# Performance work log

Hardware: AMD Instinct MI355X
Metric: run time of the kernel (lower is better)

The kernel has to match this reference:

```python
import jax, jax.numpy as jnp
import numpy as np

NUM_BOXES = 16384
NUM_CLASS = 3
CODE_SIZE = 7
NMS_PRE = 1024
NMS_POST = 512
NMS_THRESH = 0.8
EPS = 1e-8


def _cross(a, b):
    return a[..., 0] * b[..., 1] - a[..., 1] * b[..., 0]


def _bev_corners(b5):
    # b5: (..., 5) = (cx, cy, dx, dy, ry) -> corners (..., 4, 2)
    c, s = jnp.cos(b5[..., 4]), jnp.sin(b5[..., 4])
    off = jnp.array([[0.5, 0.5], [-0.5, 0.5], [-0.5, -0.5], [0.5, -0.5]], dtype=b5.dtype)
    lx = b5[..., 2:3] * off[:, 0]  # (..., 4)
    ly = b5[..., 3:4] * off[:, 1]
    cx = b5[..., 0:1] + lx * c[..., None] - ly * s[..., None]
    cy = b5[..., 1:2] + lx * s[..., None] + ly * c[..., None]
    return jnp.stack([cx, cy], axis=-1)


def _points_in_box(p, b5):
    # p: (..., K, 2), b5: (..., 5) -> (..., K) bool (point inside rotated rect)
    c, s = jnp.cos(b5[..., 4:5]), jnp.sin(b5[..., 4:5])
    rel = p - b5[..., None, 0:2]
    qx = rel[..., 0] * c + rel[..., 1] * s
    qy = -rel[..., 0] * s + rel[..., 1] * c
    return (jnp.abs(qx) <= b5[..., 2:3] * 0.5 + 1e-5) & (jnp.abs(qy) <= b5[..., 3:4] * 0.5 + 1e-5)


def _pairwise_bev_iou(b5):
    # b5: (N, 5) -> (N, N) rotated BEV IoU (matches iou3d nms_gpu's BEV IoU)
    a = b5[:, None, :]
    b = b5[None, :, :]
    ca = _bev_corners(a)  # (N,1,4,2)
    cb = _bev_corners(b)  # (1,N,4,2)
    # edge-edge segment intersections: (N,N,4,4)
    a0, da = ca, jnp.roll(ca, -1, axis=-2) - ca
    b0, db = cb, jnp.roll(cb, -1, axis=-2) - cb
    A0, DA = a0[..., :, None, :], da[..., :, None, :]
    B0, DB = b0[..., None, :, :], db[..., None, :, :]
    den = _cross(DA, DB)
    d = B0 - A0
    den_s = jnp.where(jnp.abs(den) > EPS, den, 1.0)
    t = _cross(d, DB) / den_s
    u = _cross(d, DA) / den_s
    ok = (jnp.abs(den) > EPS) & (t >= 0) & (t <= 1) & (u >= 0) & (u <= 1)
    p_ee = A0 + t[..., None] * DA  # (N,N,4,4,2)
    shp = p_ee.shape[:-3]
    p_ee = p_ee.reshape(shp + (16, 2))
    ok = ok.reshape(shp + (16,))
    in_b = _points_in_box(ca, b)  # corners of A inside B: (N,N,4)
    in_a = _points_in_box(cb, a)  # corners of B inside A: (N,N,4)
    pts = jnp.concatenate([p_ee,
                           jnp.broadcast_to(ca, shp + (4, 2)),
                           jnp.broadcast_to(cb, shp + (4, 2))], axis=-2)  # (N,N,24,2)
    msk = jnp.concatenate([ok, in_b, in_a], axis=-1)  # (N,N,24)
    # order candidate vertices by angle around centroid (intersection is convex)
    cnt = jnp.maximum(msk.sum(-1, keepdims=True), 1)
    ctr = (pts * msk[..., None]).sum(-2, keepdims=True) / cnt[..., None]  # (N,N,1,2)
    ang = jnp.arctan2(pts[..., 1] - ctr[..., 1], pts[..., 0] - ctr[..., 0])
    ang = jnp.where(msk, ang, 1e9)  # invalid points sorted to the end
    order = jnp.argsort(ang, axis=-1)
    pts_s = jnp.take_along_axis(pts, order[..., None], axis=-2)
    msk_s = jnp.take_along_axis(msk, order, axis=-1)
    first = pts_s[..., 0:1, :]
    poly = jnp.where(msk_s[..., None], pts_s, first)  # pad with first vertex (zero shoelace contribution)
    inter = 0.5 * jnp.abs(_cross(poly, jnp.roll(poly, -1, axis=-2)).sum(-1))
    area_a = a[..., 2] * a[..., 3]
    area_b = b[..., 2] * b[..., 3]
    return inter / jnp.maximum(area_a + area_b - inter, 1e-6)


def _greedy_nms(iou, thresh):
    n = iou.shape[0]
    idx = jnp.arange(n)

    def body(i, supp):
        alive = jnp.logical_not(supp[i])
        return supp | (alive & (iou[i] > thresh) & (idx > i))

    supp = jax.lax.fori_loop(0, n, body, jnp.zeros((n,), dtype=bool))
    return ~supp


def _select_one(box_preds, cls_preds):
    # box_preds: (M, 7), cls_preds: (M, C) -> padded selected indices + validity
    scores = jnp.max(cls_preds, axis=1)
    _, top_idx = jax.lax.top_k(scores, NMS_PRE)  # score-descending, like torch.topk
    bev = box_preds[top_idx][:, jnp.array([0, 1, 3, 4, 6])]  # (cx,cy,dx,dy,ry)
    iou = _pairwise_bev_iou(bev)
    keep = _greedy_nms(iou, NMS_THRESH)
    pri = jnp.where(keep, jnp.arange(NMS_PRE), 2 * NMS_PRE)
    pos = jnp.sort(pri)[:NMS_POST]  # kept positions in score order
    valid = pos < NMS_PRE
    sel = top_idx[jnp.minimum(pos, NMS_PRE - 1)]
    return sel, valid


def setup_inputs() -> dict:
    key = jax.random.key(0)
    k1, k2, k3, k4, k5 = jax.random.split(key, 5)
    B = 2
    xy = jax.random.uniform(k1, (B, NUM_BOXES, 2), minval=-50.0, maxval=50.0)
    z = jax.random.uniform(k2, (B, NUM_BOXES, 1), minval=-2.0, maxval=1.0)
    dims = jax.random.uniform(k3, (B, NUM_BOXES, 3), minval=1.0, maxval=5.0)
    ry = jax.random.uniform(k4, (B, NUM_BOXES, 1), minval=-np.pi, maxval=np.pi)
    batch_box_preds = jnp.concatenate([xy, z, dims, ry], axis=-1).astype(jnp.float32)
    batch_cls_preds = (jax.random.normal(k5, (B, NUM_BOXES, NUM_CLASS)) * 3.0).astype(jnp.float32)
    return {"batch_box_preds": batch_box_preds, "batch_cls_preds": batch_cls_preds}


def reference(batch_box_preds, batch_cls_preds):
    # RoIHeadTemplate.proposal_layer: per-sample max-score, class-agnostic NMS,
    # scatter into zero-padded (B, NMS_POST, ...) tensors.
    sel, valid = jax.vmap(_select_one)(batch_box_preds, batch_cls_preds)  # (B, NMS_POST)
    rois = jnp.take_along_axis(batch_box_preds, sel[..., None], axis=1)
    logits = jnp.take_along_axis(batch_cls_preds, sel[..., None], axis=1)
    labels = jnp.argmax(logits, axis=-1)
    scores = jnp.max(logits, axis=-1)
    v = valid[..., None]
    rois = jnp.where(v, rois, 0.0)
    logits = jnp.where(v, logits, 0.0)
    scores = jnp.where(valid, scores, 0.0)
    roi_labels = jnp.where(valid, labels, 0) + 1  # padded slots end up as 1, same as torch (zeros + 1)
    return rois, scores, roi_labels, logits
```

## Files before the change

kernel.cpp:

```cpp
#include <hip/hip_runtime.h>
#include <hip/hip_bf16.h>
#include <math.h>

#define NBOX   16384
#define NPRE   1024
#define NPOST  512
#define NMS_TH 0.8f
#define DEN_EPS 1e-8f
#define NCAND  2048
#define NBUCK  8192
#define SEGCAP 16384
#define HITS_LDS 2048
#define HSPILL  (1u << 19)

typedef unsigned long long ull;

__device__ __forceinline__ unsigned mono_f32(float a) {
  unsigned u = __float_as_uint(a);
  return (u & 0x80000000u) ? ~u : (u | 0x80000000u);
}

__global__ __launch_bounds__(256) void k_sel(
    const float* __restrict__ cls, ull* __restrict__ cand,
    unsigned* __restrict__ candCnt) {
  __shared__ unsigned hist[NBUCK];
  __shared__ unsigned smallu[8];
  __shared__ unsigned thrT, cntL;
  const int b = blockIdx.x >> 3, s = blockIdx.x & 7;
  const int t = threadIdx.x;
  const int lane = t & 63, wv = t >> 6;
  const float* cb = cls + (size_t)b * NBOX * 3;

#pragma unroll
  for (int k = 0; k < NBUCK / 256; ++k) hist[t + k * 256] = 0u;
  if (t == 0) cntL = 0u;
  __syncthreads();

  for (int k = 0; k < 64; ++k) {
    int i = k * 256 + t;
    float sc = fmaxf(cb[i * 3], fmaxf(cb[i * 3 + 1], cb[i * 3 + 2]));
    atomicAdd(&hist[mono_f32(sc) >> 19], 1u);
  }
  __syncthreads();

  unsigned csum = 0;
#pragma unroll 8
  for (int k = 0; k < 32; ++k) csum += hist[t * 32 + k];
  unsigned v = csum;
#pragma unroll
  for (int off = 1; off < 64; off <<= 1) {
    unsigned o = __shfl_down((int)v, off, 64);
    if (lane + off < 64) v += o;
  }
  if (lane == 0) smallu[wv] = v;
  __syncthreads();
  unsigned shi = 0;
  for (int w2 = wv + 1; w2 < 4; ++w2) shi += smallu[w2];
  unsigned incl = v + shi;
  unsigned safter = incl - csum;
  if (safter < NPRE && incl >= NPRE) {
    unsigned c = safter;
    for (int k = 31; k >= 0; --k) {
      c += hist[t * 32 + k];
      if (c >= NPRE) { thrT = (unsigned)(t * 32 + k); break; }
    }
  }
  __syncthreads();
  unsigned T = thrT;

  ull* seg = cand + ((size_t)b * 8 + s) * 2048;
  for (int k = s * 8; k < s * 8 + 8; ++k) {
    int i = k * 256 + t;
    float sc = fmaxf(cb[i * 3], fmaxf(cb[i * 3 + 1], cb[i * 3 + 2]));
    unsigned u = mono_f32(sc);
    bool cnd = (u >> 19) >= T;
    ull bal = __ballot(cnd);
    if (bal) {
      unsigned base = 0;
      if (lane == 0) base = atomicAdd(&cntL, (unsigned)__popcll(bal));
      base = (unsigned)__shfl((int)base, 0, 64);
      if (cnd) {
        unsigned pos = base + (unsigned)__popcll(bal & ((1ull << lane) - 1ull));
        seg[pos] = (((ull)u) << 14) | (ull)(16383 - i);
      }
    }
  }
  __syncthreads();
  if (t == 0) candCnt[b * 8 + s] = cntL;
}

__global__ __launch_bounds__(256) void k_rank(
    const float* __restrict__ box, const ull* __restrict__ cand,
    const unsigned* __restrict__ candCnt,
    int* __restrict__ topi, float* __restrict__ binfo, float4* __restrict__ pinfoG) {
  __shared__ ull candL[NCAND];
  __shared__ unsigned offs[9];
  const int b = blockIdx.x >> 3, g = blockIdx.x & 7;
  const int t = threadIdx.x;

  if (t == 0) {
    unsigned o = 0;
    for (int s = 0; s < 8; ++s) {
      offs[s] = o;
      unsigned c = candCnt[b * 8 + s];
      o += (c < 2048u) ? c : 2048u;
    }
    offs[8] = o;
  }
  __syncthreads();
  unsigned C = offs[8]; if (C > NCAND) C = NCAND;
  for (int s = 0; s < 8; ++s) {
    unsigned base = offs[s], cnt = offs[s + 1] - offs[s];
    const ull* seg = cand + ((size_t)b * 8 + s) * 2048;
    for (unsigned e = (unsigned)t; e < cnt; e += 256) {
      unsigned dst = base + e;
      if (dst < NCAND) candL[dst] = seg[e];
    }
  }
  if (t < 2 && C + t < NCAND) candL[C + t] = 0ull;
  __syncthreads();

  int j = g * 256 + t;
  ull my = ((unsigned)j < C) ? candL[j] : 0ull;
  int r = 0;
  int kmax = (int)((C + 1) >> 1);
  const ulonglong2* p2 = (const ulonglong2*)candL;
  for (int k = 0; k < kmax; ++k) {
    ulonglong2 kk = p2[k];
    r += (kk.x > my) ? 1 : 0;
    r += (kk.y > my) ? 1 : 0;
  }
  if ((unsigned)j >= C || r >= NPRE) return;
  int i = 16383 - (int)(my & 0x3FFFULL);
  topi[b * NPRE + r] = i;
  const float* bp = box + ((size_t)b * NBOX + i) * 7;
  float x = bp[0], y = bp[1], dx = bp[3], dy = bp[4], ry = bp[6];
  float c = cosf(ry), s = sinf(ry);
  float* o = binfo + ((size_t)b * NPRE + r) * 16;
  o[0] = x; o[1] = y; o[2] = dx; o[3] = dy; o[4] = c; o[5] = s;
  const float offx[4] = {0.5f, -0.5f, -0.5f, 0.5f};
  const float offy[4] = {0.5f, 0.5f, -0.5f, -0.5f};
#pragma unroll
  for (int k = 0; k < 4; ++k) {
    float lx = dx * offx[k], ly = dy * offy[k];
    o[6 + k]  = x + lx * c - ly * s;
    o[10 + k] = y + lx * s + ly * c;
  }
  float rad = 0.5f * sqrtf(dx * dx + dy * dy);
  float area = dx * dy;
  o[14] = rad; o[15] = area;
  pinfoG[(size_t)b * NPRE + r] = make_float4(x, y, rad, area);
}

__global__ __launch_bounds__(256) void k_pairs(
    const float4* __restrict__ pinfoG, unsigned* __restrict__ wl,
    unsigned* __restrict__ wlcnt) {
  __shared__ float4 pin[NPRE];
  __shared__ unsigned cntW;
  const int b = blockIdx.x >> 6, blk = blockIdx.x & 63;
  const int t = threadIdx.x;
  const int lane = t & 63, wv = t >> 6;
#pragma unroll
  for (int k = 0; k < 4; ++k) pin[k * 256 + t] = pinfoG[(size_t)b * NPRE + k * 256 + t];
  if (t == 0) cntW = 0u;
  __syncthreads();

  unsigned sbase = ((unsigned)b * 64 + (unsigned)blk) * SEGCAP;
  for (int iter = 0; iter < 64; ++iter) {
    int task = iter * 4 + wv;
    int q = task >> 4, w = task & 15;
    int i = q * 64 + blk;
    if (w * 64 + 63 <= i) continue;
    int j = w * 64 + lane;
    float4 pi = pin[i];
    float4 pj = pin[j];
    bool cnd = false;
    if (j > i) {
      float ddx = pi.x - pj.x, ddy = pi.y - pj.y;
      float rr = pi.z + pj.z + 1e-3f;
      if (ddx * ddx + ddy * ddy <= rr * rr) {
        float mn = fminf(pi.w, pj.w), mx = fmaxf(pi.w, pj.w);
        if (mn > NMS_TH * mx) cnd = true;
      }
    }
    ull bal = __ballot(cnd);
    if (!bal) continue;
    unsigned base = 0;
    if (lane == 0) base = atomicAdd(&cntW, (unsigned)__popcll(bal));
    base = (unsigned)__shfl((int)base, 0, 64);
    if (cnd) {
      unsigned off = base + (unsigned)__popcll(bal & ((1ull << lane) - 1ull));
      wl[sbase + off] = ((unsigned)i << 10) | (unsigned)j;
    }
  }
  __syncthreads();
  if (t == 0) wlcnt[b * 64 + blk] = cntW;
}

__device__ bool iou_exact_gt(const float* __restrict__ Ab, const float* __restrict__ Bb) {
  float ax = Ab[0], ay = Ab[1], bx = Bb[0], by = Bb[1];
  float aA = Ab[15], aB = Bb[15];
  float acx[4], acy[4], bcx[4], bcy[4];
#pragma unroll
  for (int k = 0; k < 4; ++k) {
    acx[k] = Ab[6 + k]; acy[k] = Ab[10 + k];
    bcx[k] = Bb[6 + k]; bcy[k] = Bb[10 + k];
  }
  float px[24], py[24];
  bool act[24];
#pragma unroll
  for (int p = 0; p < 4; ++p) {
    float A0x = acx[p], A0y = acy[p];
    float DAx = acx[(p + 1) & 3] - A0x, DAy = acy[(p + 1) & 3] - A0y;
#pragma unroll
    for (int q = 0; q < 4; ++q) {
      float B0x = bcx[q], B0y = bcy[q];
      float DBx = bcx[(q + 1) & 3] - B0x, DBy = bcy[(q + 1) & 3] - B0y;
      float den = DAx * DBy - DAy * DBx;
      float dxx = B0x - A0x, dyy = B0y - A0y;
      bool dok = fabsf(den) > DEN_EPS;
      float dens = dok ? den : 1.0f;
      float t = (dxx * DBy - dyy * DBx) / dens;
      float u = (dxx * DAy - dyy * DAx) / dens;
      int k = p * 4 + q;
      px[k] = A0x + t * DAx;
      py[k] = A0y + t * DAy;
      act[k] = dok && t >= 0.f && t <= 1.f && u >= 0.f && u <= 1.f;
    }
  }
  float cA = Ab[4], sA = Ab[5], cB = Bb[4], sB = Bb[5];
#pragma unroll
  for (int k = 0; k < 4; ++k) {
    float rx = acx[k] - bx, ry = acy[k] - by;
    float qx =  rx * cB + ry * sB, qy = -rx * sB + ry * cB;
    px[16 + k] = acx[k]; py[16 + k] = acy[k];
    act[16 + k] = (fabsf(qx) <= Bb[2] * 0.5f + 1e-5f) && (fabsf(qy) <= Bb[3] * 0.5f + 1e-5f);
  }
#pragma unroll
  for (int k = 0; k < 4; ++k) {
    float rx = bcx[k] - ax, ry = bcy[k] - ay;
    float qx =  rx * cA + ry * sA, qy = -rx * sA + ry * cA;
    px[20 + k] = bcx[k]; py[20 + k] = bcy[k];
    act[20 + k] = (fabsf(qx) <= Ab[2] * 0.5f + 1e-5f) && (fabsf(qy) <= Ab[3] * 0.5f + 1e-5f);
  }
  int cnt = 0; float sx = 0.f, sy = 0.f;
#pragma unroll
  for (int k = 0; k < 24; ++k)
    if (act[k]) { cnt++; sx += px[k]; sy += py[k]; }
  float fc = (float)(cnt > 1 ? cnt : 1);
  float cx0 = sx / fc, cy0 = sy / fc;
  ull key[24];
#pragma unroll
  for (int k = 0; k < 24; ++k) {
    float ang = atan2f(py[k] - cy0, px[k] - cx0);
    key[k] = act[k] ? ((((ull)mono_f32(ang)) << 5) | (ull)k) : ~0ull;
  }
  ull kmin = ~0ull; float fx = 0.f, fy = 0.f;
#pragma unroll
  for (int k = 0; k < 24; ++k) {
    bool lt = key[k] < kmin;
    kmin = lt ? key[k] : kmin;
    fx = lt ? px[k] : fx;
    fy = lt ? py[k] : fy;
  }
  float ssum = 0.f;
#pragma unroll
  for (int k = 0; k < 24; ++k) {
    ull myk = key[k];
    ull best = ~0ull; float nx = fx, ny = fy;
#pragma unroll
    for (int j = 0; j < 24; ++j) {
      bool c = (key[j] > myk) && (key[j] < best);
      best = c ? key[j] : best;
      nx = c ? px[j] : nx;
      ny = c ? py[j] : ny;
    }
    float contrib = px[k] * ny - py[k] * nx;
    ssum += (myk != ~0ull) ? contrib : 0.f;
  }
  float inter = 0.5f * fabsf(ssum);
  float uni = aA + aB - inter;
  return inter / fmaxf(uni, 1e-6f) > NMS_TH;
}

__device__ __forceinline__ int popbelow(const unsigned* rowbm, int i) {
  int s = 0, w = i >> 5;
  for (int k = 0; k < w; ++k) s += __popc(rowbm[k]);
  s += __popc(rowbm[w] & ((1u << (i & 31)) - 1u));
  return s;
}

__global__ __launch_bounds__(512) void k_fin(
    const float* __restrict__ box, const float* __restrict__ cls,
    const int* __restrict__ topi, const float* __restrict__ binfo,
    const unsigned* __restrict__ wl, const unsigned* __restrict__ wlcnt,
    unsigned* __restrict__ hspill, float* __restrict__ out, int B) {
  __shared__ unsigned maskL[128 * 32];
  __shared__ unsigned hitsL[HITS_LDS];
  __shared__ unsigned rlist[NPRE];
  __shared__ unsigned segoff[65];
  __shared__ unsigned rowbm[32];
  __shared__ ull remv_sh[16];
  __shared__ unsigned smallu[8];
  __shared__ unsigned hcnt, rn_sh;

  const int b = blockIdx.x, t = threadIdx.x;
  const int lane = t & 63, wv = t >> 6;

  for (int k = t; k < 128 * 32; k += 512) maskL[k] = 0u;
  if (t < 32) rowbm[t] = 0u;
  if (t == 0) {
    hcnt = 0u;
    unsigned o = 0;
    for (int s = 0; s < 64; ++s) {
      segoff[s] = o;
      unsigned c = wlcnt[b * 64 + s];
      o += (c < (unsigned)SEGCAP) ? c : (unsigned)SEGCAP;
    }
    segoff[64] = o;
  }
  __syncthreads();

  const float* bi = binfo + (size_t)b * NPRE * 16;
  unsigned W = segoff[64];
  for (unsigned e = (unsigned)t; e < W; e += 512) {
    int lo = 0, hi = 63;
    while (lo < hi) {
      int mid = (lo + hi + 1) >> 1;
      if (segoff[mid] <= e) lo = mid; else hi = mid - 1;
    }
    unsigned pk = wl[((size_t)b * 64 + lo) * SEGCAP + (e - segoff[lo])];
    unsigned i = pk >> 10, j = pk & 1023u;
    if (iou_exact_gt(bi + (size_t)i * 16, bi + (size_t)j * 16)) {
      unsigned h = atomicAdd(&hcnt, 1u);
      if (h < HITS_LDS) hitsL[h] = pk;
      else if (h < HITS_LDS + HSPILL) hspill[(size_t)b * HSPILL + (h - HITS_LDS)] = pk;
      atomicOr(&rowbm[i >> 5], 1u << (i & 31));
    }
  }
  __syncthreads();

  for (int row = t; row < NPRE; row += 512) {
    if ((rowbm[row >> 5] >> (row & 31)) & 1u)
      rlist[popbelow(rowbm, row)] = (unsigned)row;
  }
  if (t == 0) {
    unsigned s = 0;
    for (int w = 0; w < 32; ++w) s += (unsigned)__popc(rowbm[w]);
    rn_sh = s;
  }
  __syncthreads();
  unsigned H = hcnt; if (H > HITS_LDS + HSPILL) H = HITS_LDS + HSPILL;
  for (unsigned h = (unsigned)t; h < H; h += 512) {
    unsigned pk = (h < HITS_LDS) ? hitsL[h] : hspill[(size_t)b * HSPILL + (h - HITS_LDS)];
    unsigned i = pk >> 10, j = pk & 1023u;
    int slot = popbelow(rowbm, (int)i);
    if (slot < 128) atomicOr(&maskL[slot * 32 + (j >> 5)], 1u << (j & 31));
  }
  __syncthreads();

  if (wv == 0) {
    ull remv = 0;
    unsigned rn = rn_sh;
    for (unsigned s = 0; s < rn; ++s) {
      unsigned row = rlist[s];
      ull m = 0;
      if (s < 128) {
        if (lane < 16)
          m = (ull)maskL[s * 32 + lane * 2] | ((ull)maskL[s * 32 + lane * 2 + 1] << 32);
      } else {
        for (unsigned h = 0; h < H; ++h) {
          unsigned pk = (h < HITS_LDS) ? hitsL[h] : hspill[(size_t)b * HSPILL + (h - HITS_LDS)];
          if ((pk >> 10) == row) {
            unsigned j = pk & 1023u;
            if (lane == (int)(j >> 6)) m |= 1ull << (j & 63);
          }
        }
      }
      ull rw = __shfl(remv, (int)(row >> 6), 64);
      if (!((rw >> (row & 63)) & 1ULL)) remv |= m;
    }
    if (lane < 16) remv_sh[lane] = remv;
  }
  __syncthreads();

  int p0 = t * 2;
  ull rw = remv_sh[p0 >> 6];
  int a0 = ((rw >> (p0 & 63)) & 1ULL) ? 0 : 1;
  int a1 = ((rw >> ((p0 + 1) & 63)) & 1ULL) ? 0 : 1;
  int myc = a0 + a1;
  int v = myc;
#pragma unroll
  for (int off = 1; off < 64; off <<= 1) {
    int t2 = __shfl_up(v, off, 64);
    if (lane >= off) v += t2;
  }
  if (lane == 63) smallu[wv] = (unsigned)v;
  __syncthreads();
  int pre = 0;
  for (int w2 = 0; w2 < wv; ++w2) pre += (int)smallu[w2];
  int total = 0;
  for (int w2 = 0; w2 < 8; ++w2) total += (int)smallu[w2];
  int s = pre + v - myc;

  float* rois   = out;
  float* scores = out + (size_t)B * NPOST * 7;
  float* labels = scores + (size_t)B * NPOST;
  float* logits = labels + (size_t)B * NPOST;
  int aa[2] = {a0, a1};
#pragma unroll
  for (int k = 0; k < 2; ++k) {
    if (aa[k] && s < NPOST) {
      int orig = topi[b * NPRE + p0 + k];
      const float* bb = box + ((size_t)b * NBOX + orig) * 7;
      float* ro = rois + ((size_t)b * NPOST + s) * 7;
#pragma unroll
      for (int c2 = 0; c2 < 7; ++c2) ro[c2] = bb[c2];
      const float* cc = cls + ((size_t)b * NBOX + orig) * 3;
      float l0 = cc[0], l1 = cc[1], l2 = cc[2];
      float m = fmaxf(l0, fmaxf(l1, l2));
      int lab = (l0 == m) ? 0 : ((l1 == m) ? 1 : 2);
      scores[b * NPOST + s] = m;
      labels[b * NPOST + s] = (float)(lab + 1);
      float* lg = logits + ((size_t)b * NPOST + s) * 3;
      lg[0] = l0; lg[1] = l1; lg[2] = l2;
    }
    s += aa[k];
  }
  if (t < NPOST && t >= total) {
    float* ro = rois + ((size_t)b * NPOST + t) * 7;
#pragma unroll
    for (int c2 = 0; c2 < 7; ++c2) ro[c2] = 0.f;
    scores[b * NPOST + t] = 0.f;
    labels[b * NPOST + t] = 1.f;
    float* lg = logits + ((size_t)b * NPOST + t) * 3;
    lg[0] = 0.f; lg[1] = 0.f; lg[2] = 0.f;
  }
}

extern "C" void kernel_launch(void* const* d_in, const int* in_sizes, int n_in,
                              void* d_out, int out_size, void* d_ws, size_t ws_size,
                              hipStream_t stream) {
  const float* box = (const float*)d_in[0];
  const float* cls = (const float*)d_in[1];
  float* out = (float*)d_out;
  int B = in_sizes[0] / (NBOX * 7);

  char* w = (char*)d_ws;
  size_t off = 0;
  ull* cand        = (ull*)(w + off);      off += (size_t)B * 8 * 2048 * sizeof(ull);
  unsigned* candCt = (unsigned*)(w + off); off += (size_t)B * 8 * sizeof(unsigned);
  int* topi        = (int*)(w + off);      off += (size_t)B * NPRE * sizeof(int);
  unsigned* wlcnt  = (unsigned*)(w + off); off += (size_t)B * 64 * sizeof(unsigned);
  off = (off + 63) & ~(size_t)63;
  float* binfo     = (float*)(w + off);    off += (size_t)B * NPRE * 16 * sizeof(float);
  float4* pinfoG   = (float4*)(w + off);   off += (size_t)B * NPRE * sizeof(float4);
  unsigned* wl     = (unsigned*)(w + off); off += (size_t)B * 64 * SEGCAP * sizeof(unsigned);
  unsigned* hspill = (unsigned*)(w + off); off += (size_t)B * HSPILL * sizeof(unsigned);
  (void)off; (void)ws_size; (void)out_size; (void)n_in;

  hipLaunchKernelGGL(k_sel,   dim3(B * 8),  dim3(256), 0, stream, cls, cand, candCt);
  hipLaunchKernelGGL(k_rank,  dim3(B * 8),  dim3(256), 0, stream, box, cand, candCt, topi, binfo, pinfoG);
  hipLaunchKernelGGL(k_pairs, dim3(B * 64), dim3(256), 0, stream, pinfoG, wl, wlcnt);
  hipLaunchKernelGGL(k_fin,   dim3(B),      dim3(512), 0, stream, box, cls, topi, binfo, wl, wlcnt, hspill, out, B);
}
```

Measured before the change: 147.7 us.

## Move exact rotated IoU evaluation from per-sample finish kernel into parallel pair kernel

The exact polygon IoU test for candidate pairs now runs in k_pairs, spread over B*64 blocks, instead of in k_fin, which has only one 512-thread block per sample. Candidates are buffered in LDS and evaluated after the scan, and only confirmed hits are written to per-segment global lists. k_fin then reads those hit segments through a binary search over segment offsets to build the row bitmap and suppression masks. The cost is more LDS and register pressure in k_pairs, plus repeated binary searches and global reads in k_fin's fallback path.

```diff
diff --git a/kernel.cpp b/kernel.cpp
--- a/kernel.cpp
+++ b/kernel.cpp
@@ -10,8 +10,7 @@
 #define NCAND  2048
 #define NBUCK  8192
 #define SEGCAP 16384
-#define HITS_LDS 2048
-#define HSPILL  (1u << 19)
+#define CANDL  2048
 
 typedef unsigned long long ull;
 
@@ -152,19 +151,107 @@
   pinfoG[(size_t)b * NPRE + r] = make_float4(x, y, rad, area);
 }
 
+__device__ bool iou_exact_gt(const float* __restrict__ Ab, const float* __restrict__ Bb) {
+  float ax = Ab[0], ay = Ab[1], bx = Bb[0], by = Bb[1];
+  float aA = Ab[15], aB = Bb[15];
+  float acx[4], acy[4], bcx[4], bcy[4];
+#pragma unroll
+  for (int k = 0; k < 4; ++k) {
+    acx[k] = Ab[6 + k]; acy[k] = Ab[10 + k];
+    bcx[k] = Bb[6 + k]; bcy[k] = Bb[10 + k];
+  }
+  float px[24], py[24];
+  bool act[24];
+#pragma unroll
+  for (int p = 0; p < 4; ++p) {
+    float A0x = acx[p], A0y = acy[p];
+    float DAx = acx[(p + 1) & 3] - A0x, DAy = acy[(p + 1) & 3] - A0y;
+#pragma unroll
+    for (int q = 0; q < 4; ++q) {
+      float B0x = bcx[q], B0y = bcy[q];
+      float DBx = bcx[(q + 1) & 3] - B0x, DBy = bcy[(q + 1) & 3] - B0y;
+      float den = DAx * DBy - DAy * DBx;
+      float dxx = B0x - A0x, dyy = B0y - A0y;
+      bool dok = fabsf(den) > DEN_EPS;
+      float dens = dok ? den : 1.0f;
+      float t = (dxx * DBy - dyy * DBx) / dens;
+      float u = (dxx * DAy - dyy * DAx) / dens;
+      int k = p * 4 + q;
+      px[k] = A0x + t * DAx;
+      py[k] = A0y + t * DAy;
+      act[k] = dok && t >= 0.f && t <= 1.f && u >= 0.f && u <= 1.f;
+    }
+  }
+  float cA = Ab[4], sA = Ab[5], cB = Bb[4], sB = Bb[5];
+#pragma unroll
+  for (int k = 0; k < 4; ++k) {
+    float rx = acx[k] - bx, ry = acy[k] - by;
+    float qx =  rx * cB + ry * sB, qy = -rx * sB + ry * cB;
+    px[16 + k] = acx[k]; py[16 + k] = acy[k];
+    act[16 + k] = (fabsf(qx) <= Bb[2] * 0.5f + 1e-5f) && (fabsf(qy) <= Bb[3] * 0.5f + 1e-5f);
+  }
+#pragma unroll
+  for (int k = 0; k < 4; ++k) {
+    float rx = bcx[k] - ax, ry = bcy[k] - ay;
+    float qx =  rx * cA + ry * sA, qy = -rx * sA + ry * cA;
+    px[20 + k] = bcx[k]; py[20 + k] = bcy[k];
+    act[20 + k] = (fabsf(qx) <= Ab[2] * 0.5f + 1e-5f) && (fabsf(qy) <= Ab[3] * 0.5f + 1e-5f);
+  }
+  int cnt = 0; float sx = 0.f, sy = 0.f;
+#pragma unroll
+  for (int k = 0; k < 24; ++k)
+    if (act[k]) { cnt++; sx += px[k]; sy += py[k]; }
+  float fc = (float)(cnt > 1 ? cnt : 1);
+  float cx0 = sx / fc, cy0 = sy / fc;
+  ull key[24];
+#pragma unroll
+  for (int k = 0; k < 24; ++k) {
+    float ang = atan2f(py[k] - cy0, px[k] - cx0);
+    key[k] = act[k] ? ((((ull)mono_f32(ang)) << 5) | (ull)k) : ~0ull;
+  }
+  ull kmin = ~0ull; float fx = 0.f, fy = 0.f;
+#pragma unroll
+  for (int k = 0; k < 24; ++k) {
+    bool lt = key[k] < kmin;
+    kmin = lt ? key[k] : kmin;
+    fx = lt ? px[k] : fx;
+    fy = lt ? py[k] : fy;
+  }
+  float ssum = 0.f;
+#pragma unroll
+  for (int k = 0; k < 24; ++k) {
+    ull myk = key[k];
+    ull best = ~0ull; float nx = fx, ny = fy;
+#pragma unroll
+    for (int j = 0; j < 24; ++j) {
+      bool c = (key[j] > myk) && (key[j] < best);
+      best = c ? key[j] : best;
+      nx = c ? px[j] : nx;
+      ny = c ? py[j] : ny;
+    }
+    float contrib = px[k] * ny - py[k] * nx;
+    ssum += (myk != ~0ull) ? contrib : 0.f;
+  }
+  float inter = 0.5f * fabsf(ssum);
+  float uni = aA + aB - inter;
+  return inter / fmaxf(uni, 1e-6f) > NMS_TH;
+}
+
 __global__ __launch_bounds__(256) void k_pairs(
-    const float4* __restrict__ pinfoG, unsigned* __restrict__ wl,
-    unsigned* __restrict__ wlcnt) {
+    const float4* __restrict__ pinfoG, const float* __restrict__ binfo,
+    unsigned* __restrict__ hitseg, unsigned* __restrict__ hitcnt) {
   __shared__ float4 pin[NPRE];
-  __shared__ unsigned cntW;
+  __shared__ unsigned candL[CANDL];
+  __shared__ unsigned cntC, cntH;
   const int b = blockIdx.x >> 6, blk = blockIdx.x & 63;
   const int t = threadIdx.x;
   const int lane = t & 63, wv = t >> 6;
 #pragma unroll
   for (int k = 0; k < 4; ++k) pin[k * 256 + t] = pinfoG[(size_t)b * NPRE + k * 256 + t];
-  if (t == 0) cntW = 0u;
-  __syncthreads();
-
+  if (t == 0) { cntC = 0u; cntH = 0u; }
+  __syncthreads();
+
+  const float* bi = binfo + (size_t)b * NPRE * 16;
   unsigned sbase = ((unsigned)b * 64 + (unsigned)blk) * SEGCAP;
   for (int iter = 0; iter < 64; ++iter) {
     int task = iter * 4 + wv;
@@ -186,101 +273,33 @@
     ull bal = __ballot(cnd);
     if (!bal) continue;
     unsigned base = 0;
-    if (lane == 0) base = atomicAdd(&cntW, (unsigned)__popcll(bal));
+    if (lane == 0) base = atomicAdd(&cntC, (unsigned)__popcll(bal));
     base = (unsigned)__shfl((int)base, 0, 64);
     if (cnd) {
       unsigned off = base + (unsigned)__popcll(bal & ((1ull << lane) - 1ull));
-      wl[sbase + off] = ((unsigned)i << 10) | (unsigned)j;
-    }
-  }
-  __syncthreads();
-  if (t == 0) wlcnt[b * 64 + blk] = cntW;
-}
-
-__device__ bool iou_exact_gt(const float* __restrict__ Ab, const float* __restrict__ Bb) {
-  float ax = Ab[0], ay = Ab[1], bx = Bb[0], by = Bb[1];
-  float aA = Ab[15], aB = Bb[15];
-  float acx[4], acy[4], bcx[4], bcy[4];
-#pragma unroll
-  for (int k = 0; k < 4; ++k) {
-    acx[k] = Ab[6 + k]; acy[k] = Ab[10 + k];
-    bcx[k] = Bb[6 + k]; bcy[k] = Bb[10 + k];
-  }
-  float px[24], py[24];
-  bool act[24];
-#pragma unroll
-  for (int p = 0; p < 4; ++p) {
-    float A0x = acx[p], A0y = acy[p];
-    float DAx = acx[(p + 1) & 3] - A0x, DAy = acy[(p + 1) & 3] - A0y;
-#pragma unroll
-    for (int q = 0; q < 4; ++q) {
-      float B0x = bcx[q], B0y = bcy[q];
-      float DBx = bcx[(q + 1) & 3] - B0x, DBy = bcy[(q + 1) & 3] - B0y;
-      float den = DAx * DBy - DAy * DBx;
-      float dxx = B0x - A0x, dyy = B0y - A0y;
-      bool dok = fabsf(den) > DEN_EPS;
-      float dens = dok ? den : 1.0f;
-      float t = (dxx * DBy - dyy * DBx) / dens;
-      float u = (dxx * DAy - dyy * DAx) / dens;
-      int k = p * 4 + q;
-      px[k] = A0x + t * DAx;
-      py[k] = A0y + t * DAy;
-      act[k] = dok && t >= 0.f && t <= 1.f && u >= 0.f && u <= 1.f;
-    }
-  }
-  float cA = Ab[4], sA = Ab[5], cB = Bb[4], sB = Bb[5];
-#pragma unroll
-  for (int k = 0; k < 4; ++k) {
-    float rx = acx[k] - bx, ry = acy[k] - by;
-    float qx =  rx * cB + ry * sB, qy = -rx * sB + ry * cB;
-    px[16 + k] = acx[k]; py[16 + k] = acy[k];
-    act[16 + k] = (fabsf(qx) <= Bb[2] * 0.5f + 1e-5f) && (fabsf(qy) <= Bb[3] * 0.5f + 1e-5f);
-  }
-#pragma unroll
-  for (int k = 0; k < 4; ++k) {
-    float rx = bcx[k] - ax, ry = bcy[k] - ay;
-    float qx =  rx * cA + ry * sA, qy = -rx * sA + ry * cA;
-    px[20 + k] = bcx[k]; py[20 + k] = bcy[k];
-    act[20 + k] = (fabsf(qx) <= Ab[2] * 0.5f + 1e-5f) && (fabsf(qy) <= Ab[3] * 0.5f + 1e-5f);
-  }
-  int cnt = 0; float sx = 0.f, sy = 0.f;
-#pragma unroll
-  for (int k = 0; k < 24; ++k)
-    if (act[k]) { cnt++; sx += px[k]; sy += py[k]; }
-  float fc = (float)(cnt > 1 ? cnt : 1);
-  float cx0 = sx / fc, cy0 = sy / fc;
-  ull key[24];
-#pragma unroll
-  for (int k = 0; k < 24; ++k) {
-    float ang = atan2f(py[k] - cy0, px[k] - cx0);
-    key[k] = act[k] ? ((((ull)mono_f32(ang)) << 5) | (ull)k) : ~0ull;
-  }
-  ull kmin = ~0ull; float fx = 0.f, fy = 0.f;
-#pragma unroll
-  for (int k = 0; k < 24; ++k) {
-    bool lt = key[k] < kmin;
-    kmin = lt ? key[k] : kmin;
-    fx = lt ? px[k] : fx;
-    fy = lt ? py[k] : fy;
-  }
-  float ssum = 0.f;
-#pragma unroll
-  for (int k = 0; k < 24; ++k) {
-    ull myk = key[k];
-    ull best = ~0ull; float nx = fx, ny = fy;
-#pragma unroll
-    for (int j = 0; j < 24; ++j) {
-      bool c = (key[j] > myk) && (key[j] < best);
-      best = c ? key[j] : best;
-      nx = c ? px[j] : nx;
-      ny = c ? py[j] : ny;
-    }
-    float contrib = px[k] * ny - py[k] * nx;
-    ssum += (myk != ~0ull) ? contrib : 0.f;
-  }
-  float inter = 0.5f * fabsf(ssum);
-  float uni = aA + aB - inter;
-  return inter / fmaxf(uni, 1e-6f) > NMS_TH;
+      unsigned pk = ((unsigned)i << 10) | (unsigned)j;
+      if (off < CANDL) candL[off] = pk;
+      else {
+        if (iou_exact_gt(bi + (size_t)i * 16, bi + (size_t)j * 16)) {
+          unsigned h = atomicAdd(&cntH, 1u);
+          hitseg[sbase + h] = pk;
+        }
+      }
+    }
+  }
+  __syncthreads();
+
+  unsigned C = cntC; if (C > CANDL) C = CANDL;
+  for (unsigned e = (unsigned)t; e < C; e += 256) {
+    unsigned pk = candL[e];
+    unsigned i = pk >> 10, j = pk & 1023u;
+    if (iou_exact_gt(bi + (size_t)i * 16, bi + (size_t)j * 16)) {
+      unsigned h = atomicAdd(&cntH, 1u);
+      hitseg[sbase + h] = pk;
+    }
+  }
+  __syncthreads();
+  if (t == 0) hitcnt[b * 64 + blk] = (cntH < (unsigned)SEGCAP) ? cntH : (unsigned)SEGCAP;
 }
 
 __device__ __forceinline__ int popbelow(const unsigned* rowbm, int i) {
@@ -292,17 +311,15 @@
 
 __global__ __launch_bounds__(512) void k_fin(
     const float* __restrict__ box, const float* __restrict__ cls,
-    const int* __restrict__ topi, const float* __restrict__ binfo,
-    const unsigned* __restrict__ wl, const unsigned* __restrict__ wlcnt,
-    unsigned* __restrict__ hspill, float* __restrict__ out, int B) {
+    const int* __restrict__ topi, const unsigned* __restrict__ hitseg,
+    const unsigned* __restrict__ hitcnt, float* __restrict__ out, int B) {
   __shared__ unsigned maskL[128 * 32];
-  __shared__ unsigned hitsL[HITS_LDS];
   __shared__ unsigned rlist[NPRE];
   __shared__ unsigned segoff[65];
   __shared__ unsigned rowbm[32];
   __shared__ ull remv_sh[16];
   __shared__ unsigned smallu[8];
-  __shared__ unsigned hcnt, rn_sh;
+  __shared__ unsigned rn_sh;
 
   const int b = blockIdx.x, t = threadIdx.x;
   const int lane = t & 63, wv = t >> 6;
@@ -310,36 +327,24 @@
   for (int k = t; k < 128 * 32; k += 512) maskL[k] = 0u;
   if (t < 32) rowbm[t] = 0u;
   if (t == 0) {
-    hcnt = 0u;
     unsigned o = 0;
     for (int s = 0; s < 64; ++s) {
       segoff[s] = o;
-      unsigned c = wlcnt[b * 64 + s];
+      unsigned c = hitcnt[b * 64 + s];
       o += (c < (unsigned)SEGCAP) ? c : (unsigned)SEGCAP;
     }
     segoff[64] = o;
   }
   __syncthreads();
-
-  const float* bi = binfo + (size_t)b * NPRE * 16;
-  unsigned W = segoff[64];
-  for (unsigned e = (unsigned)t; e < W; e += 512) {
+  unsigned H = segoff[64];
+
+  for (unsigned e = (unsigned)t; e < H; e += 512) {
     int lo = 0, hi = 63;
-    while (lo < hi) {
-      int mid = (lo + hi + 1) >> 1;
-      if (segoff[mid] <= e) lo = mid; else hi = mid - 1;
-    }
-    unsigned pk = wl[((size_t)b * 64 + lo) * SEGCAP + (e - segoff[lo])];
-    unsigned i = pk >> 10, j = pk & 1023u;
-    if (iou_exact_gt(bi + (size_t)i * 16, bi + (size_t)j * 16)) {
-      unsigned h = atomicAdd(&hcnt, 1u);
-      if (h < HITS_LDS) hitsL[h] = pk;
-      else if (h < HITS_LDS + HSPILL) hspill[(size_t)b * HSPILL + (h - HITS_LDS)] = pk;
-      atomicOr(&rowbm[i >> 5], 1u << (i & 31));
-    }
-  }
-  __syncthreads();
-
+    while (lo < hi) { int mid = (lo + hi + 1) >> 1; if (segoff[mid] <= e) lo = mid; else hi = mid - 1; }
+    unsigned pk = hitseg[((size_t)b * 64 + lo) * SEGCAP + (e - segoff[lo])];
+    atomicOr(&rowbm[(pk >> 10) >> 5], 1u << ((pk >> 10) & 31));
+  }
+  __syncthreads();
   for (int row = t; row < NPRE; row += 512) {
     if ((rowbm[row >> 5] >> (row & 31)) & 1u)
       rlist[popbelow(rowbm, row)] = (unsigned)row;
@@ -350,9 +355,10 @@
     rn_sh = s;
   }
   __syncthreads();
-  unsigned H = hcnt; if (H > HITS_LDS + HSPILL) H = HITS_LDS + HSPILL;
-  for (unsigned h = (unsigned)t; h < H; h += 512) {
-    unsigned pk = (h < HITS_LDS) ? hitsL[h] : hspill[(size_t)b * HSPILL + (h - HITS_LDS)];
+  for (unsigned e = (unsigned)t; e < H; e += 512) {
+    int lo = 0, hi = 63;
+    while (lo < hi) { int mid = (lo + hi + 1) >> 1; if (segoff[mid] <= e) lo = mid; else hi = mid - 1; }
+    unsigned pk = hitseg[((size_t)b * 64 + lo) * SEGCAP + (e - segoff[lo])];
     unsigned i = pk >> 10, j = pk & 1023u;
     int slot = popbelow(rowbm, (int)i);
     if (slot < 128) atomicOr(&maskL[slot * 32 + (j >> 5)], 1u << (j & 31));
@@ -369,8 +375,10 @@
         if (lane < 16)
           m = (ull)maskL[s * 32 + lane * 2] | ((ull)maskL[s * 32 + lane * 2 + 1] << 32);
       } else {
-        for (unsigned h = 0; h < H; ++h) {
-          unsigned pk = (h < HITS_LDS) ? hitsL[h] : hspill[(size_t)b * HSPILL + (h - HITS_LDS)];
+        for (unsigned e = 0; e < H; ++e) {
+          int lo = 0, hi = 63;
+          while (lo < hi) { int mid = (lo + hi + 1) >> 1; if (segoff[mid] <= e) lo = mid; else hi = mid - 1; }
+          unsigned pk = hitseg[((size_t)b * 64 + lo) * SEGCAP + (e - segoff[lo])];
           if ((pk >> 10) == row) {
             unsigned j = pk & 1023u;
             if (lane == (int)(j >> 6)) m |= 1ull << (j & 63);
@@ -451,16 +459,15 @@
   ull* cand        = (ull*)(w + off);      off += (size_t)B * 8 * 2048 * sizeof(ull);
   unsigned* candCt = (unsigned*)(w + off); off += (size_t)B * 8 * sizeof(unsigned);
   int* topi        = (int*)(w + off);      off += (size_t)B * NPRE * sizeof(int);
-  unsigned* wlcnt  = (unsigned*)(w + off); off += (size_t)B * 64 * sizeof(unsigned);
+  unsigned* hitcnt = (unsigned*)(w + off); off += (size_t)B * 64 * sizeof(unsigned);
   off = (off + 63) & ~(size_t)63;
   float* binfo     = (float*)(w + off);    off += (size_t)B * NPRE * 16 * sizeof(float);
   float4* pinfoG   = (float4*)(w + off);   off += (size_t)B * NPRE * sizeof(float4);
-  unsigned* wl     = (unsigned*)(w + off); off += (size_t)B * 64 * SEGCAP * sizeof(unsigned);
-  unsigned* hspill = (unsigned*)(w + off); off += (size_t)B * HSPILL * sizeof(unsigned);
+  unsigned* hitseg = (unsigned*)(w + off); off += (size_t)B * 64 * SEGCAP * sizeof(unsigned);
   (void)off; (void)ws_size; (void)out_size; (void)n_in;
 
   hipLaunchKernelGGL(k_sel,   dim3(B * 8),  dim3(256), 0, stream, cls, cand, candCt);
   hipLaunchKernelGGL(k_rank,  dim3(B * 8),  dim3(256), 0, stream, box, cand, candCt, topi, binfo, pinfoG);
-  hipLaunchKernelGGL(k_pairs, dim3(B * 64), dim3(256), 0, stream, pinfoG, wl, wlcnt);
-  hipLaunchKernelGGL(k_fin,   dim3(B),      dim3(512), 0, stream, box, cls, topi, binfo, wl, wlcnt, hspill, out, B);
-}
+  hipLaunchKernelGGL(k_pairs, dim3(B * 64), dim3(256), 0, stream, pinfoG, binfo, hitseg, hitcnt);
+  hipLaunchKernelGGL(k_fin,   dim3(B),      dim3(512), 0, stream, box, cls, topi, hitseg, hitcnt, out, B);
+}
```

Result: faster. 132.0 us (-10.6%).
